# Kernel tuning notes

Hardware: AMD Instinct MI355X
Metric: run time of the kernel (lower is better)

The kernel has to match this reference:

```python
import jax, jax.numpy as jnp
import numpy as np

MIN_DISTANCE = 2.9
LOSS_WEIGHT = 1.0

def setup_inputs() -> dict:
    key = jax.random.key(0)
    coordinates = jax.random.normal(key, (64, 3072), dtype=jnp.float32) * 5.0
    return {"coordinates": coordinates}

def reference(coordinates) -> jnp.ndarray:
    B, C = coordinates.shape
    N = C // 3
    atoms = coordinates.reshape(B, N, 3)
    # pairwise squared distances: [B, N, N]
    diff = atoms[:, :, None, :] - atoms[:, None, :, :]
    dist_sq = jnp.sum(diff * diff, axis=-1)
    dist = jnp.sqrt(dist_sq + 1e-8)
    # strict upper-triangular mask (i < j), same for every batch element
    i = jnp.arange(N)
    triu = (i[:, None] < i[None, :]).astype(dist.dtype)  # [N, N]
    violations = jnp.maximum(MIN_DISTANCE - dist, 0.0) * triu
    total_loss = jnp.sum(violations * violations)
    return LOSS_WEIGHT * total_loss / B
```

## Files before the change

### kernel.cpp

```cpp
#include <hip/hip_runtime.h>


constexpr int   NA      = 1024;
constexpr int   NB      = 64;
constexpr int   JCH     = 128;
constexpr int   THREADS = 256;
constexpr int   IPT     = 2;
constexpr int   ICH     = THREADS * IPT;
constexpr int   GRID_I  = NA / ICH;
constexpr int   GRID_J  = NA / JCH;
constexpr int   NPART   = NB * GRID_I * GRID_J;
constexpr float MIN_D   = 2.9f;

__global__ __launch_bounds__(THREADS, 4)
void pair_kernel(const float* __restrict__ coords, float* __restrict__ partials)
{
    const int b   = blockIdx.x;
    const int ic  = blockIdx.y;
    const int jc  = blockIdx.z;
    const int tid = threadIdx.x;

    __shared__ float sj[JCH * 3];

    const float* cb = coords + (size_t)b * (NA * 3);
    const float* cj = cb + jc * (JCH * 3);

    sj[tid] = cj[tid];
    if (tid < JCH * 3 - THREADS) sj[THREADS + tid] = cj[THREADS + tid];

    const int i0 = ic * ICH + tid;
    const int i1 = i0 + THREADS;
    const float x0 = cb[3*i0+0], y0 = cb[3*i0+1], z0 = cb[3*i0+2];
    const float x1 = cb[3*i1+0], y1 = cb[3*i1+1], z1 = cb[3*i1+2];

    __syncthreads();

    float acc0 = 0.f, acc1 = 0.f;
    #pragma unroll 8
    for (int j = 0; j < JCH; ++j) {
        const float xj = sj[3*j+0], yj = sj[3*j+1], zj = sj[3*j+2];
        {
            const float dx = x0-xj, dy = y0-yj, dz = z0-zj;
            const float ds = fmaf(dx,dx, fmaf(dy,dy, fmaf(dz,dz, 1e-8f)));
            const float v  = fmaxf(MIN_D - __builtin_amdgcn_sqrtf(ds), 0.f);
            acc0 = fmaf(v, v, acc0);
        }
        {
            const float dx = x1-xj, dy = y1-yj, dz = z1-zj;
            const float ds = fmaf(dx,dx, fmaf(dy,dy, fmaf(dz,dz, 1e-8f)));
            const float v  = fmaxf(MIN_D - __builtin_amdgcn_sqrtf(ds), 0.f);
            acc1 = fmaf(v, v, acc1);
        }
    }
    float acc = acc0 + acc1;

    #pragma unroll
    for (int off = 1; off < 64; off <<= 1)
        acc += __shfl_xor(acc, off, 64);

    __shared__ float wsum[THREADS / 64];
    if ((tid & 63) == 0) wsum[tid >> 6] = acc;
    __syncthreads();
    if (tid == 0) {
        float s = 0.f;
        #pragma unroll
        for (int w = 0; w < THREADS / 64; ++w) s += wsum[w];
        partials[(b * GRID_I + ic) * GRID_J + jc] = s;
    }
}

__global__ __launch_bounds__(256)
void reduce_kernel(const float* __restrict__ partials, float* __restrict__ out)
{
    const int tid = threadIdx.x;
    float s = 0.f;
    #pragma unroll
    for (int k = tid; k < NPART; k += 256) s += partials[k];
    #pragma unroll
    for (int off = 1; off < 64; off <<= 1)
        s += __shfl_xor(s, off, 64);
    __shared__ float wsum[4];
    if ((tid & 63) == 0) wsum[tid >> 6] = s;
    __syncthreads();
    if (tid == 0) {
        float tot = (wsum[0] + wsum[1]) + (wsum[2] + wsum[3]);
        const float d0 = __builtin_amdgcn_sqrtf(1e-8f);
        const float v0 = fmaxf(MIN_D - d0, 0.f);
        const float cd = v0 * v0;
        tot -= (float)(NB * NA) * cd;
        out[0] = tot * (0.5f / (float)NB);
    }
}

extern "C" void kernel_launch(void* const* d_in, const int* in_sizes, int n_in,
                              void* d_out, int out_size, void* d_ws, size_t ws_size,
                              hipStream_t stream)
{
    const float* coords = (const float*)d_in[0];
    float* partials = (float*)d_ws;
    float* out = (float*)d_out;

    dim3 grid(NB, GRID_I, GRID_J);
    pair_kernel<<<grid, THREADS, 0, stream>>>(coords, partials);
    reduce_kernel<<<1, 256, 0, stream>>>(partials, out);
}
```

Baseline: 74.00 us.

## Compute only upper-triangular tile pairs instead of full symmetric matrix

Replaces the full N×N pairwise evaluation (later halved and diagonal-corrected) with a grid over upper-triangular tile pairs plus diagonal tiles handled with a circular offset scheme. This roughly halves the sqrt/FMA work per batch. Shared memory switches to float4 atom records for vectorised LDS reads. The diagonal blocks add a masked, non-unrolled loop, and the larger number of smaller blocks increases per-block overhead.

Measured after the change: 68.57 us. -7.3%, faster.

```diff
diff --git a/kernel.cpp b/kernel.cpp
--- a/kernel.cpp
+++ b/kernel.cpp
@@ -1,71 +1,83 @@
 #include <hip/hip_runtime.h>
 
 
-constexpr int   NA      = 1024;
-constexpr int   NB      = 64;
-constexpr int   JCH     = 128;
-constexpr int   THREADS = 256;
-constexpr int   IPT     = 2;
-constexpr int   ICH     = THREADS * IPT;
-constexpr int   GRID_I  = NA / ICH;
-constexpr int   GRID_J  = NA / JCH;
-constexpr int   NPART   = NB * GRID_I * GRID_J;
-constexpr float MIN_D   = 2.9f;
+constexpr int   NA     = 1024;
+constexpr int   NB     = 64;
+constexpr int   TILE   = 128;
+constexpr int   NT     = NA / TILE;
+constexpr int   NCROSS = NT * (NT - 1) / 2;
+constexpr int   NPAIR  = NCROSS + NT;
+constexpr int   NPART  = NB * NPAIR;
+constexpr float MIN_D  = 2.9f;
 
-__global__ __launch_bounds__(THREADS, 4)
+static __device__ const int TI_[NCROSS] = {
+    0,0,0,0,0,0,0, 1,1,1,1,1,1, 2,2,2,2,2, 3,3,3,3, 4,4,4, 5,5, 6};
+static __device__ const int TJ_[NCROSS] = {
+    1,2,3,4,5,6,7, 2,3,4,5,6,7, 3,4,5,6,7, 4,5,6,7, 5,6,7, 6,7, 7};
+
+__global__ __launch_bounds__(256, 4)
 void pair_kernel(const float* __restrict__ coords, float* __restrict__ partials)
 {
-    const int b   = blockIdx.x;
-    const int ic  = blockIdx.y;
-    const int jc  = blockIdx.z;
-    const int tid = threadIdx.x;
+    const int b = blockIdx.x;
+    const int p = blockIdx.y;
+    const int t = threadIdx.x;
+    const int l = t & 127;
+    const int h = t >> 7;
 
-    __shared__ float sj[JCH * 3];
+    __shared__ float4 sj[TILE];
 
     const float* cb = coords + (size_t)b * (NA * 3);
-    const float* cj = cb + jc * (JCH * 3);
 
-    sj[tid] = cj[tid];
-    if (tid < JCH * 3 - THREADS) sj[THREADS + tid] = cj[THREADS + tid];
+    const bool diag = (p >= NCROSS);
+    const int ti = diag ? (p - NCROSS) : TI_[p];
+    const int tj = diag ? (p - NCROSS) : TJ_[p];
 
-    const int i0 = ic * ICH + tid;
-    const int i1 = i0 + THREADS;
-    const float x0 = cb[3*i0+0], y0 = cb[3*i0+1], z0 = cb[3*i0+2];
-    const float x1 = cb[3*i1+0], y1 = cb[3*i1+1], z1 = cb[3*i1+2];
+    if (t < TILE) {
+        const int ja = tj * TILE + t;
+        sj[t] = make_float4(cb[3*ja+0], cb[3*ja+1], cb[3*ja+2], 0.f);
+    }
+
+    const int i = ti * TILE + l;
+    const float xi = cb[3*i+0], yi = cb[3*i+1], zi = cb[3*i+2];
 
     __syncthreads();
 
-    float acc0 = 0.f, acc1 = 0.f;
-    #pragma unroll 8
-    for (int j = 0; j < JCH; ++j) {
-        const float xj = sj[3*j+0], yj = sj[3*j+1], zj = sj[3*j+2];
-        {
-            const float dx = x0-xj, dy = y0-yj, dz = z0-zj;
+    float acc = 0.f;
+    if (!diag) {
+        const int j0 = h * 64;
+        #pragma unroll 8
+        for (int jj = 0; jj < 64; ++jj) {
+            const float4 a = sj[j0 + jj];
+            const float dx = xi - a.x, dy = yi - a.y, dz = zi - a.z;
             const float ds = fmaf(dx,dx, fmaf(dy,dy, fmaf(dz,dz, 1e-8f)));
             const float v  = fmaxf(MIN_D - __builtin_amdgcn_sqrtf(ds), 0.f);
-            acc0 = fmaf(v, v, acc0);
+            acc = fmaf(v, v, acc);
         }
-        {
-            const float dx = x1-xj, dy = y1-yj, dz = z1-zj;
+    } else {
+        const int d0 = h ? 65 : 1;
+        const int nd = h ? 63 : 64;
+        for (int k = 0; k < nd; ++k) {
+            const int jj = l + d0 + k;
+            const float4 a = sj[jj & (TILE - 1)];
+            const float dx = xi - a.x, dy = yi - a.y, dz = zi - a.z;
             const float ds = fmaf(dx,dx, fmaf(dy,dy, fmaf(dz,dz, 1e-8f)));
             const float v  = fmaxf(MIN_D - __builtin_amdgcn_sqrtf(ds), 0.f);
-            acc1 = fmaf(v, v, acc1);
+            float c = v * v;
+            if (jj >= TILE) c = 0.f;
+            acc += c;
         }
     }
-    float acc = acc0 + acc1;
 
     #pragma unroll
     for (int off = 1; off < 64; off <<= 1)
         acc += __shfl_xor(acc, off, 64);
 
-    __shared__ float wsum[THREADS / 64];
-    if ((tid & 63) == 0) wsum[tid >> 6] = acc;
+    __shared__ float wsum[4];
+    if ((t & 63) == 0) wsum[t >> 6] = acc;
     __syncthreads();
-    if (tid == 0) {
-        float s = 0.f;
-        #pragma unroll
-        for (int w = 0; w < THREADS / 64; ++w) s += wsum[w];
-        partials[(b * GRID_I + ic) * GRID_J + jc] = s;
+    if (t == 0) {
+        const float s = (wsum[0] + wsum[1]) + (wsum[2] + wsum[3]);
+        partials[b * NPAIR + p] = s;
     }
 }
 
@@ -74,7 +86,6 @@
 {
     const int tid = threadIdx.x;
     float s = 0.f;
-    #pragma unroll
     for (int k = tid; k < NPART; k += 256) s += partials[k];
     #pragma unroll
     for (int off = 1; off < 64; off <<= 1)
@@ -83,12 +94,8 @@
     if ((tid & 63) == 0) wsum[tid >> 6] = s;
     __syncthreads();
     if (tid == 0) {
-        float tot = (wsum[0] + wsum[1]) + (wsum[2] + wsum[3]);
-        const float d0 = __builtin_amdgcn_sqrtf(1e-8f);
-        const float v0 = fmaxf(MIN_D - d0, 0.f);
-        const float cd = v0 * v0;
-        tot -= (float)(NB * NA) * cd;
-        out[0] = tot * (0.5f / (float)NB);
+        const float tot = (wsum[0] + wsum[1]) + (wsum[2] + wsum[3]);
+        out[0] = tot * (1.0f / (float)NB);
     }
 }
 
@@ -100,7 +107,7 @@
     float* partials = (float*)d_ws;
     float* out = (float*)d_out;
 
-    dim3 grid(NB, GRID_I, GRID_J);
-    pair_kernel<<<grid, THREADS, 0, stream>>>(coords, partials);
+    dim3 grid(NB, NPAIR);
+    pair_kernel<<<grid, 256, 0, stream>>>(coords, partials);
     reduce_kernel<<<1, 256, 0, stream>>>(partials, out);
 }
```
